# Kernel tuning notes

Measured on AMD Instinct MI355X. Metric: run time of the kernel, lower is better.

## Reference

```python
import jax, jax.numpy as jnp
import numpy as np

FEATURE_DIM = 128
B = 1024
N_CLASSES = 16


def setup_inputs() -> dict:
    key = jax.random.key(0)
    k1, k2, k3, k4, k5, k6 = jax.random.split(key, 6)
    D = FEATURE_DIM
    features = jax.random.normal(k1, (B, D), dtype=jnp.float32)
    labels = jax.random.randint(k2, (B,), 0, N_CLASSES, dtype=jnp.int64)
    # edge_network params: Linear(2D -> D), ReLU, Linear(D -> 1), Sigmoid
    s1 = 1.0 / np.sqrt(2 * D)
    s2 = 1.0 / np.sqrt(D)
    W1 = jax.random.uniform(k3, (2 * D, D), jnp.float32, -s1, s1)
    b1 = jax.random.uniform(k4, (D,), jnp.float32, -s1, s1)
    w2 = jax.random.uniform(k5, (D,), jnp.float32, -s2, s2)
    b2 = jax.random.uniform(k6, (), jnp.float32, -s2, s2)
    return {"features": features, "labels": labels, "W1": W1, "b1": b1,
            "w2": w2, "b2": b2}


def reference(features, labels, W1, b1, w2, b2):
    D = features.shape[1]
    # Concat-linear split: cat([f_i, f_j]) @ W1 == f_i @ W1[:D] + f_j @ W1[D:]
    hi = features @ W1[:D]          # [B, D] contribution of node i
    hj = features @ W1[D:]          # [B, D] contribution of node j
    h = jax.nn.relu(hi[:, None, :] + hj[None, :, :] + b1)   # [B, B, D]
    score = jax.nn.sigmoid(h @ w2 + b2)                      # [B, B]
    n = features.shape[0]
    off_diag = ~jnp.eye(n, dtype=bool)
    same_label = labels[:, None] == labels[None, :]
    mask = off_diag & same_label
    return jnp.where(mask, score, jnp.zeros_like(score))
```

## Files before the change

### kernel.cpp

```cpp
#include <hip/hip_runtime.h>

#define FD 128
#define NB 1024
#define NC 16
#define NCB (NC * 16)
#define MAXM 112
#define CKCAP 28
#define LDP 132

__global__ __launch_bounds__(256) void eg_one(
    const float* __restrict__ f, const int* __restrict__ labels,
    const float* __restrict__ W1, const float* __restrict__ b1,
    const float* __restrict__ w2, const float* __restrict__ b2,
    float* __restrict__ out)
{
  const int bid = blockIdx.x;
  const int tid = threadIdx.x;

  if (bid >= NCB) {
    const int i = bid - NCB;
    const int li = labels[i];
    float* __restrict__ row = out + (size_t)i * NB;
#pragma unroll
    for (int q = 0; q < 4; ++q) {
      const int j = tid + q * 256;
      if (labels[j] != li) row[j] = 0.f;
    }
    return;
  }

  __shared__ __align__(16) float lds[2 * CKCAP * LDP];
  __shared__ int mem[MAXM];
  __shared__ int mcnt;
  float (*fs)[LDP]  = reinterpret_cast<float (*)[LDP]>(lds);
  float (*his)[LDP] = reinterpret_cast<float (*)[LDP]>(lds);
  float (*hjs)[LDP] = reinterpret_cast<float (*)[LDP]>(lds + CKCAP * LDP);

  const int c  = bid >> 4;
  const int qi = (bid >> 2) & 3;
  const int qj = bid & 3;

  if (tid < 64) {
    const int lane = tid;
    int base = 0;
    for (int w = 0; w < 16; ++w) {
      const int j = w * 64 + lane;
      const bool fl = (labels[j] == c);
      const unsigned long long msk = __ballot(fl);
      const int pos = base + __popcll(msk & ((1ull << lane) - 1ull));
      if (fl && pos < MAXM) mem[pos] = j;
      base += __popcll(msk);
    }
    if (lane == 0) mcnt = base < MAXM ? base : MAXM;
  }
  __syncthreads();

  const int m  = mcnt;
  const int ck = (m + 3) >> 2;
  const int i0 = qi * ck;
  const int SI = max(0, min(m, i0 + ck) - i0);
  const int j0 = qj * ck;
  const int SJ = max(0, min(m, j0 + ck) - j0);
  const int R  = SI + SJ;

  for (int idx = tid; idx < R * 32; idx += 256) {
    const int r  = idx >> 5;
    const int fo = (idx & 31) << 2;
    const int g  = (r < SI) ? mem[i0 + r] : mem[j0 + (r - SI)];
    *reinterpret_cast<float4*>(&fs[r][fo]) =
        *reinterpret_cast<const float4*>(f + g * FD + fo);
  }
  __syncthreads();

  const int half  = tid >> 7;
  const int r8    = (tid >> 4) & 7;
  const int dg    = (tid & 15) << 3;
  const int S     = half ? SJ : SI;
  const int rbase = half ? SI : 0;

  float acc[4][8];
  {
    float4 bA = make_float4(0.f, 0.f, 0.f, 0.f), bB = bA;
    if (!half) {
      bA = *reinterpret_cast<const float4*>(b1 + dg);
      bB = *reinterpret_cast<const float4*>(b1 + dg + 4);
    }
#pragma unroll
    for (int rr = 0; rr < 4; ++rr) {
      acc[rr][0] = bA.x; acc[rr][1] = bA.y; acc[rr][2] = bA.z; acc[rr][3] = bA.w;
      acc[rr][4] = bB.x; acc[rr][5] = bB.y; acc[rr][6] = bB.z; acc[rr][7] = bB.w;
    }
  }
  const float* frow[4];
#pragma unroll
  for (int rr = 0; rr < 4; ++rr) {
    const int r = r8 + rr * 8;
    frow[rr] = fs[rbase + (r < S ? r : 0)];
  }
  const float* __restrict__ Wp = W1 + half * FD * FD + dg;
#pragma unroll 4
  for (int k = 0; k < FD; ++k) {
    const float4 wA = *reinterpret_cast<const float4*>(Wp + k * FD);
    const float4 wB = *reinterpret_cast<const float4*>(Wp + k * FD + 4);
#pragma unroll
    for (int rr = 0; rr < 4; ++rr) {
      const float fv = frow[rr][k];
      acc[rr][0] = fmaf(fv, wA.x, acc[rr][0]);
      acc[rr][1] = fmaf(fv, wA.y, acc[rr][1]);
      acc[rr][2] = fmaf(fv, wA.z, acc[rr][2]);
      acc[rr][3] = fmaf(fv, wA.w, acc[rr][3]);
      acc[rr][4] = fmaf(fv, wB.x, acc[rr][4]);
      acc[rr][5] = fmaf(fv, wB.y, acc[rr][5]);
      acc[rr][6] = fmaf(fv, wB.z, acc[rr][6]);
      acc[rr][7] = fmaf(fv, wB.w, acc[rr][7]);
    }
  }
  __syncthreads();

#pragma unroll
  for (int rr = 0; rr < 4; ++rr) {
    const int r = r8 + rr * 8;
    if (r < S) {
      float* dst = (half ? hjs[r] : his[r]) + dg;
      *reinterpret_cast<float4*>(dst) =
          make_float4(acc[rr][0], acc[rr][1], acc[rr][2], acc[rr][3]);
      *reinterpret_cast<float4*>(dst + 4) =
          make_float4(acc[rr][4], acc[rr][5], acc[rr][6], acc[rr][7]);
    }
  }
  __syncthreads();

  const int wv = tid >> 6, lane = tid & 63;
  const int a = lane >> 3, b = lane & 7;
  const int nti = (SI + 7) >> 3, ntj = (SJ + 7) >> 3;
  const float bb = b2[0];
  for (int t = wv; t < nti * ntj; t += 4) {
    const int ti = t / ntj, tj = t - ti * ntj;
    const int ii = ti * 8 + a, jj = tj * 8 + b;
    const int ic = ii < SI ? ii : SI - 1;
    const int jc = jj < SJ ? jj : SJ - 1;
    float acc2 = 0.f;
#pragma unroll 8
    for (int d = 0; d < FD; d += 4) {
      const float4 hv = *reinterpret_cast<const float4*>(&his[ic][d]);
      const float4 gv = *reinterpret_cast<const float4*>(&hjs[jc][d]);
      const float4 w4 = *reinterpret_cast<const float4*>(&w2[d]);
      acc2 = fmaf(fmaxf(hv.x + gv.x, 0.f), w4.x, acc2);
      acc2 = fmaf(fmaxf(hv.y + gv.y, 0.f), w4.y, acc2);
      acc2 = fmaf(fmaxf(hv.z + gv.z, 0.f), w4.z, acc2);
      acc2 = fmaf(fmaxf(hv.w + gv.w, 0.f), w4.w, acc2);
    }
    if (ii < SI && jj < SJ) {
      const int gi = mem[i0 + ii], gj = mem[j0 + jj];
      out[(size_t)gi * NB + gj] =
          (gi == gj) ? 0.f : 1.f / (1.f + __expf(-(acc2 + bb)));
    }
  }
}

extern "C" void kernel_launch(void* const* d_in, const int* in_sizes, int n_in,
                              void* d_out, int out_size, void* d_ws, size_t ws_size,
                              hipStream_t stream) {
  const float* f      = (const float*)d_in[0];
  const int*   labels = (const int*)d_in[1];
  const float* W1     = (const float*)d_in[2];
  const float* b1     = (const float*)d_in[3];
  const float* w2     = (const float*)d_in[4];
  const float* b2     = (const float*)d_in[5];
  float* out = (float*)d_out;

  eg_one<<<NCB + NB, 256, 0, stream>>>(f, labels, W1, b1, w2, b2, out);
}
```

Measured before the change: 22.96 us.

## Widen blocks to 1024 threads, one row per thread in projection stage

Raises the block size from 256 to 1024 threads. In the projection GEMM each thread now computes one row instead of four, and the pair-scoring loop strides over 16 waves. The zero-fill blocks each handle four rows, so the grid shrinks from 1280 to 512 blocks. The aim is more parallelism per class block and lower block-launch overhead, at the cost of less register reuse of W1 loads, possibly lower occupancy, and more threads idle when class chunks are small.

Result: slower. 39.64 us (+72.7%).

```diff
diff --git a/kernel.cpp b/kernel.cpp
--- a/kernel.cpp
+++ b/kernel.cpp
@@ -4,11 +4,12 @@
 #define NB 1024
 #define NC 16
 #define NCB (NC * 16)
+#define NFB 256
 #define MAXM 112
 #define CKCAP 28
 #define LDP 132
 
-__global__ __launch_bounds__(256) void eg_one(
+__global__ __launch_bounds__(1024) void eg_one(
     const float* __restrict__ f, const int* __restrict__ labels,
     const float* __restrict__ W1, const float* __restrict__ b1,
     const float* __restrict__ w2, const float* __restrict__ b2,
@@ -18,12 +19,13 @@
   const int tid = threadIdx.x;
 
   if (bid >= NCB) {
-    const int i = bid - NCB;
+    const int i = (bid - NCB) * 4 + (tid >> 8);
     const int li = labels[i];
+    const int jb = tid & 255;
     float* __restrict__ row = out + (size_t)i * NB;
 #pragma unroll
     for (int q = 0; q < 4; ++q) {
-      const int j = tid + q * 256;
+      const int j = jb + q * 256;
       if (labels[j] != li) row[j] = 0.f;
     }
     return;
@@ -63,7 +65,7 @@
   const int SJ = max(0, min(m, j0 + ck) - j0);
   const int R  = SI + SJ;
 
-  for (int idx = tid; idx < R * 32; idx += 256) {
+  for (int idx = tid; idx < R * 32; idx += 1024) {
     const int r  = idx >> 5;
     const int fo = (idx & 31) << 2;
     const int g  = (r < SI) ? mem[i0 + r] : mem[j0 + (r - SI)];
@@ -72,61 +74,43 @@
   }
   __syncthreads();
 
-  const int half  = tid >> 7;
-  const int r8    = (tid >> 4) & 7;
-  const int dg    = (tid & 15) << 3;
+  const int half = tid >> 9;
+  const int rq   = (tid >> 4) & 31;
+  const int dg   = (tid & 15) << 3;
   const int S     = half ? SJ : SI;
   const int rbase = half ? SI : 0;
+  const bool valid = rq < S;
+  const float* __restrict__ frow = fs[rbase + (valid ? rq : 0)];
 
-  float acc[4][8];
+  float acc[8];
   {
     float4 bA = make_float4(0.f, 0.f, 0.f, 0.f), bB = bA;
     if (!half) {
       bA = *reinterpret_cast<const float4*>(b1 + dg);
       bB = *reinterpret_cast<const float4*>(b1 + dg + 4);
     }
-#pragma unroll
-    for (int rr = 0; rr < 4; ++rr) {
-      acc[rr][0] = bA.x; acc[rr][1] = bA.y; acc[rr][2] = bA.z; acc[rr][3] = bA.w;
-      acc[rr][4] = bB.x; acc[rr][5] = bB.y; acc[rr][6] = bB.z; acc[rr][7] = bB.w;
-    }
-  }
-  const float* frow[4];
-#pragma unroll
-  for (int rr = 0; rr < 4; ++rr) {
-    const int r = r8 + rr * 8;
-    frow[rr] = fs[rbase + (r < S ? r : 0)];
+    acc[0] = bA.x; acc[1] = bA.y; acc[2] = bA.z; acc[3] = bA.w;
+    acc[4] = bB.x; acc[5] = bB.y; acc[6] = bB.z; acc[7] = bB.w;
   }
   const float* __restrict__ Wp = W1 + half * FD * FD + dg;
 #pragma unroll 4
   for (int k = 0; k < FD; ++k) {
     const float4 wA = *reinterpret_cast<const float4*>(Wp + k * FD);
     const float4 wB = *reinterpret_cast<const float4*>(Wp + k * FD + 4);
-#pragma unroll
-    for (int rr = 0; rr < 4; ++rr) {
-      const float fv = frow[rr][k];
-      acc[rr][0] = fmaf(fv, wA.x, acc[rr][0]);
-      acc[rr][1] = fmaf(fv, wA.y, acc[rr][1]);
-      acc[rr][2] = fmaf(fv, wA.z, acc[rr][2]);
-      acc[rr][3] = fmaf(fv, wA.w, acc[rr][3]);
-      acc[rr][4] = fmaf(fv, wB.x, acc[rr][4]);
-      acc[rr][5] = fmaf(fv, wB.y, acc[rr][5]);
-      acc[rr][6] = fmaf(fv, wB.z, acc[rr][6]);
-      acc[rr][7] = fmaf(fv, wB.w, acc[rr][7]);
-    }
+    const float fv = frow[k];
+    acc[0] = fmaf(fv, wA.x, acc[0]); acc[1] = fmaf(fv, wA.y, acc[1]);
+    acc[2] = fmaf(fv, wA.z, acc[2]); acc[3] = fmaf(fv, wA.w, acc[3]);
+    acc[4] = fmaf(fv, wB.x, acc[4]); acc[5] = fmaf(fv, wB.y, acc[5]);
+    acc[6] = fmaf(fv, wB.z, acc[6]); acc[7] = fmaf(fv, wB.w, acc[7]);
   }
   __syncthreads();
 
-#pragma unroll
-  for (int rr = 0; rr < 4; ++rr) {
-    const int r = r8 + rr * 8;
-    if (r < S) {
-      float* dst = (half ? hjs[r] : his[r]) + dg;
-      *reinterpret_cast<float4*>(dst) =
-          make_float4(acc[rr][0], acc[rr][1], acc[rr][2], acc[rr][3]);
-      *reinterpret_cast<float4*>(dst + 4) =
-          make_float4(acc[rr][4], acc[rr][5], acc[rr][6], acc[rr][7]);
-    }
+  if (valid) {
+    float* dst = (half ? hjs[rq] : his[rq]) + dg;
+    *reinterpret_cast<float4*>(dst) =
+        make_float4(acc[0], acc[1], acc[2], acc[3]);
+    *reinterpret_cast<float4*>(dst + 4) =
+        make_float4(acc[4], acc[5], acc[6], acc[7]);
   }
   __syncthreads();
 
@@ -134,7 +118,7 @@
   const int a = lane >> 3, b = lane & 7;
   const int nti = (SI + 7) >> 3, ntj = (SJ + 7) >> 3;
   const float bb = b2[0];
-  for (int t = wv; t < nti * ntj; t += 4) {
+  for (int t = wv; t < nti * ntj; t += 16) {
     const int ti = t / ntj, tj = t - ti * ntj;
     const int ii = ti * 8 + a, jj = tj * 8 + b;
     const int ic = ii < SI ? ii : SI - 1;
@@ -169,5 +153,5 @@
   const float* b2     = (const float*)d_in[5];
   float* out = (float*)d_out;
 
-  eg_one<<<NCB + NB, 256, 0, stream>>>(f, labels, W1, b1, w2, b2, out);
+  eg_one<<<NCB + NFB, 1024, 0, stream>>>(f, labels, W1, b1, w2, b2, out);
 }
```
